# Kernel optimization log

Hardware: AMD Instinct MI355X
Metric: run time of the kernel (lower is better)

Reference implementation:

```python
import jax, jax.numpy as jnp
import numpy as np

B, T, C, H = 8, 2048, 1024, 64


def build_rope_cache(seq_len, dim):
    half = dim // 2
    inv_freq = 1.0 / (10000.0 ** (jnp.arange(half, dtype=jnp.float32) / half))
    t = jnp.arange(seq_len, dtype=jnp.float32)
    freqs = t[:, None] * inv_freq[None, :]          # (T, half)
    cos = jnp.repeat(jnp.cos(freqs), 2, axis=-1)    # (T, dim) interleaved
    sin = jnp.repeat(jnp.sin(freqs), 2, axis=-1)
    return cos, sin


def apply_rope(x, cos, sin):
    # x: (B, T, H); cos/sin: (T, H)
    x1 = x[..., ::2]
    x2 = x[..., 1::2]
    rot = jnp.stack([-x2, x1], axis=-1).reshape(x.shape)
    return x * cos[None] + rot * sin[None]


def setup_inputs() -> dict:
    key = jax.random.key(0)
    kx, kq, kk, kv = jax.random.split(key, 4)
    scale = 1.0 / np.sqrt(C)
    return {
        "x": jax.random.normal(kx, (B, T, C), dtype=jnp.float32),
        "Wq": jax.random.normal(kq, (C, H), dtype=jnp.float32) * scale,
        "Wk": jax.random.normal(kk, (C, H), dtype=jnp.float32) * scale,
        "Wv": jax.random.normal(kv, (C, H), dtype=jnp.float32) * scale,
    }


def reference(x, Wq, Wk, Wv):
    Bc, Tc, _ = x.shape
    head_size = Wq.shape[1]
    cos, sin = build_rope_cache(Tc, head_size)

    q = apply_rope(x @ Wq, cos, sin)   # (B, T, H)
    k = apply_rope(x @ Wk, cos, sin)   # (B, T, H)
    v = x @ Wv                          # (B, T, H)

    # full TxT masked softmax attention (matches original non-fused path)
    wei = jnp.einsum('bth,bsh->bts', q, k) * (head_size ** -0.5)  # (B, T, T)
    causal = jnp.tril(jnp.ones((Tc, Tc), dtype=bool))
    wei = jnp.where(causal[None], wei, -jnp.inf)
    wei = jax.nn.softmax(wei, axis=-1)
    # dropout p=0 (eval mode) -> identity
    return jnp.einsum('bts,bsh->bth', wei, v)
```

## Files before the change

### kernel.cpp

```cpp
#include <hip/hip_runtime.h>
#include <cmath>

#define Tn  2048
#define Cn  1024
#define Hn  64
#define BTn 16384

typedef _Float16 f16x8 __attribute__((ext_vector_type(8)));
typedef _Float16 f16x4 __attribute__((ext_vector_type(4)));
typedef _Float16 f16x2 __attribute__((ext_vector_type(2)));
typedef float    f32x4 __attribute__((ext_vector_type(4)));

__global__ __launch_bounds__(256) void prep_w_kernel(
    const float* __restrict__ Wq, const float* __restrict__ Wk,
    const float* __restrict__ Wv, _Float16* __restrict__ Wt)
{
    __shared__ float ts[64][65];
    const int blk = blockIdx.x;
    const int p   = blk >> 4;
    const int c0  = (blk & 15) * 64;
    const float* __restrict__ W = (p == 0) ? Wq : (p == 1) ? Wk : Wv;
    const int tid = threadIdx.x;
    #pragma unroll
    for (int it = 0; it < 16; it++) {
        int idx = tid + it * 256;
        int c = idx >> 6, n = idx & 63;
        ts[c][n] = W[(size_t)(c0 + c) * Hn + n];
    }
    __syncthreads();
    #pragma unroll
    for (int it = 0; it < 16; it++) {
        int idx = tid + it * 256;
        int n = idx >> 6, c = idx & 63;
        Wt[(size_t)(p * 64 + n) * Cn + c0 + c] = (_Float16)ts[c][n];
    }
}

#define XSP 1032

__global__ __launch_bounds__(512) void proj_kernel(
    const float* __restrict__ x, const _Float16* __restrict__ Wt,
    _Float16* __restrict__ qh, _Float16* __restrict__ kh, _Float16* __restrict__ vT)
{
    __shared__ _Float16 xs[32 * XSP];
    const int row0 = blockIdx.x * 32;
    const int tid  = threadIdx.x;
    const int wave = tid >> 6, lane = tid & 63;
    const int quad = lane >> 4, l15 = lane & 15;
    const int wr = wave >> 2, wc = wave & 3;

    #pragma unroll 8
    for (int it = 0; it < 16; it++) {
        int idx = tid + it * 512;
        int r = idx >> 8, c4 = idx & 255;
        float4 xv = *(const float4*)&x[(size_t)(row0 + r) * Cn + c4 * 4];
        f16x4 hv = { (_Float16)xv.x, (_Float16)xv.y, (_Float16)xv.z, (_Float16)xv.w };
        *(f16x4*)&xs[r * XSP + c4 * 4] = hv;
    }
    __syncthreads();

    f32x4 acc[3] = {};
    const _Float16* __restrict__ wb = Wt + (size_t)(wc * 48 + l15) * Cn + quad * 8;

    #pragma unroll 4
    for (int kc = 0; kc < Cn; kc += 32) {
        f16x8 b0 = *(const f16x8*)&wb[kc];
        f16x8 b1 = *(const f16x8*)&wb[16 * Cn + kc];
        f16x8 b2 = *(const f16x8*)&wb[32 * Cn + kc];
        f16x8 a  = *(const f16x8*)&xs[(wr * 16 + l15) * XSP + kc + quad * 8];
        acc[0] = __builtin_amdgcn_mfma_f32_16x16x32_f16(a, b0, acc[0], 0, 0, 0);
        acc[1] = __builtin_amdgcn_mfma_f32_16x16x32_f16(a, b1, acc[1], 0, 0, 0);
        acc[2] = __builtin_amdgcn_mfma_f32_16x16x32_f16(a, b2, acc[2], 0, 0, 0);
    }

    const int bidx = row0 >> 11;
    #pragma unroll
    for (int nt = 0; nt < 3; nt++) {
        const int n = wc * 48 + nt * 16 + l15;
        const int p = n >> 6;
        const int h = n & 63;
        if (p < 2) {
            _Float16* __restrict__ outb = (p == 0) ? qh : kh;
            const float invf = __expf(-0.2878231366242557f * (float)(h >> 1));
            #pragma unroll
            for (int r = 0; r < 4; r++) {
                int   row = row0 + wr * 16 + quad * 4 + r;
                float val = acc[nt][r];
                float partner = __shfl_xor(val, 1, 64);
                float ang = (float)(row & (Tn - 1)) * invf;
                float sv, cv;
                __sincosf(ang, &sv, &cv);
                float res = (h & 1) ? fmaf(val, cv,  partner * sv)
                                    : fmaf(val, cv, -partner * sv);
                if (p == 0) res *= 0.125f;
                float resn = __shfl_xor(res, 1, 64);
                if (!(l15 & 1)) {
                    f16x2 pk = { (_Float16)res, (_Float16)resn };
                    *(f16x2*)&outb[(size_t)row * Hn + h] = pk;
                }
            }
        } else {
            int t = (row0 & (Tn - 1)) + wr * 16 + quad * 4;
            f16x4 pv = { (_Float16)acc[nt][0], (_Float16)acc[nt][1],
                         (_Float16)acc[nt][2], (_Float16)acc[nt][3] };
            *(f16x4*)&vT[((size_t)bidx * Hn + h) * Tn + t] = pv;
        }
    }
}

#define PSP 72

__global__ __launch_bounds__(256) void attn_kernel(
    const _Float16* __restrict__ qh, const _Float16* __restrict__ kh,
    const _Float16* __restrict__ vT, float* __restrict__ out)
{
    __shared__ _Float16 ps[4][16 * PSP];
    __shared__ float ocomb[4][16][68];
    __shared__ float mlcomb[4][2][16];

    const int blk = blockIdx.x;
    const int b   = blk & 7;
    const int j   = blk >> 3;
    const int jm  = j & 31, g = j >> 5;
    const int qt  = (g == 0) ? (127 - jm)
                  : (g == 1) ? (64 + jm)
                  : (g == 2) ? (63 - jm) : jm;
    const int t0  = qt * 16;
    const int tid = threadIdx.x;
    const int w = tid >> 6, lane = tid & 63;
    const int quad = lane >> 4, l15 = lane & 15;

    const _Float16* __restrict__ qb = qh + (size_t)b * Tn * Hn;
    const _Float16* __restrict__ kb = kh + (size_t)b * Tn * Hn;
    const _Float16* __restrict__ vb = vT + (size_t)b * Hn * Tn;

    const f16x8 aq0 = *(const f16x8*)&qb[(size_t)(t0 + l15) * Hn +      quad * 8];
    const f16x8 aq1 = *(const f16x8*)&qb[(size_t)(t0 + l15) * Hn + 32 + quad * 8];

    const _Float16 one1 = (_Float16)1.0f;
    const f16x8 onesv = { one1, one1, one1, one1, one1, one1, one1, one1 };

    float m_run[4];
    f32x4 oacc[5] = {};
    #pragma unroll
    for (int r = 0; r < 4; r++) m_run[r] = -1e30f;

    const int nst = (t0 + 16 + 63) >> 6;
    for (int jt = w; jt < nst; jt += 4) {
        const int s0 = jt * 64;

        f16x8 kf[4][2];
        #pragma unroll
        for (int nt = 0; nt < 4; nt++) {
            const _Float16* kp = &kb[(size_t)(s0 + nt * 16 + l15) * Hn + quad * 8];
            kf[nt][0] = *(const f16x8*)kp;
            kf[nt][1] = *(const f16x8*)(kp + 32);
        }
        f32x4 sacc[4];
        #pragma unroll
        for (int nt = 0; nt < 4; nt++) {
            f32x4 z = {};
            z = __builtin_amdgcn_mfma_f32_16x16x32_f16(aq0, kf[nt][0], z, 0, 0, 0);
            z = __builtin_amdgcn_mfma_f32_16x16x32_f16(aq1, kf[nt][1], z, 0, 0, 0);
            sacc[nt] = z;
        }

        f16x8 vf[2][4];
        #pragma unroll
        for (int sc = 0; sc < 2; sc++)
            #pragma unroll
            for (int ht = 0; ht < 4; ht++)
                vf[sc][ht] = *(const f16x8*)&vb[(size_t)(ht * 16 + l15) * Tn
                                                + s0 + sc * 32 + quad * 8];

        if (jt == nst - 1) {
            #pragma unroll
            for (int nt = 0; nt < 4; nt++)
                #pragma unroll
                for (int r = 0; r < 4; r++) {
                    int scol = s0 + nt * 16 + l15;
                    int trow = t0 + quad * 4 + r;
                    if (scol > trow) sacc[nt][r] = -1e30f;
                }
        }

        float pr[4][4];
        #pragma unroll
        for (int r = 0; r < 4; r++) {
            float mx = fmaxf(fmaxf(sacc[0][r], sacc[1][r]),
                             fmaxf(sacc[2][r], sacc[3][r]));
            #pragma unroll
            for (int off = 1; off < 16; off <<= 1)
                mx = fmaxf(mx, __shfl_xor(mx, off, 64));
            float mnew  = fmaxf(m_run[r], mx);
            float alpha = __expf(m_run[r] - mnew);
            m_run[r] = mnew;
            #pragma unroll
            for (int nt = 0; nt < 4; nt++)
                pr[nt][r] = __expf(sacc[nt][r] - mnew);
            #pragma unroll
            for (int ht = 0; ht < 5; ht++)
                oacc[ht][r] = oacc[ht][r] * alpha;
        }

        #pragma unroll
        for (int nt = 0; nt < 4; nt++)
            #pragma unroll
            for (int r = 0; r < 4; r++) {
                float pv = pr[nt][r];
                float pn = __shfl_xor(pv, 1, 64);
                if (!(l15 & 1)) {
                    f16x2 pk = { (_Float16)pv, (_Float16)pn };
                    *(f16x2*)&ps[w][(quad * 4 + r) * PSP + nt * 16 + l15] = pk;
                }
            }

        #pragma unroll
        for (int sc = 0; sc < 2; sc++) {
            f16x8 ap = *(const f16x8*)&ps[w][l15 * PSP + sc * 32 + quad * 8];
            #pragma unroll
            for (int ht = 0; ht < 4; ht++)
                oacc[ht] = __builtin_amdgcn_mfma_f32_16x16x32_f16(ap, vf[sc][ht],
                                                                  oacc[ht], 0, 0, 0);
            oacc[4] = __builtin_amdgcn_mfma_f32_16x16x32_f16(ap, onesv,
                                                             oacc[4], 0, 0, 0);
        }
    }

    #pragma unroll
    for (int r = 0; r < 4; r++) {
        #pragma unroll
        for (int ht = 0; ht < 4; ht++)
            ocomb[w][quad * 4 + r][ht * 16 + l15] = oacc[ht][r];
        if (l15 == 0) {
            mlcomb[w][0][quad * 4 + r] = m_run[r];
            mlcomb[w][1][quad * 4 + r] = oacc[4][r];
        }
    }
    __syncthreads();

    #pragma unroll
    for (int it = 0; it < 4; it++) {
        int idx = tid + it * 256;
        int row = idx >> 6, h = idx & 63;
        float m0 = mlcomb[0][0][row], m1 = mlcomb[1][0][row];
        float m2 = mlcomb[2][0][row], m3 = mlcomb[3][0][row];
        float mm = fmaxf(fmaxf(m0, m1), fmaxf(m2, m3));
        float a0 = __expf(m0 - mm), a1 = __expf(m1 - mm);
        float a2 = __expf(m2 - mm), a3 = __expf(m3 - mm);
        float ll = mlcomb[0][1][row] * a0 + mlcomb[1][1][row] * a1
                 + mlcomb[2][1][row] * a2 + mlcomb[3][1][row] * a3;
        float ov = ocomb[0][row][h] * a0 + ocomb[1][row][h] * a1
                 + ocomb[2][row][h] * a2 + ocomb[3][row][h] * a3;
        out[((size_t)b * Tn + t0 + row) * Hn + h] = ov / ll;
    }
}

extern "C" void kernel_launch(void* const* d_in, const int* in_sizes, int n_in,
                              void* d_out, int out_size, void* d_ws, size_t ws_size,
                              hipStream_t stream) {
    const float* x  = (const float*)d_in[0];
    const float* Wq = (const float*)d_in[1];
    const float* Wk = (const float*)d_in[2];
    const float* Wv = (const float*)d_in[3];

    const size_t qkvN = (size_t)BTn * Hn;
    _Float16* qh = (_Float16*)d_ws;
    _Float16* kh = qh + qkvN;
    _Float16* vT = kh + qkvN;
    _Float16* Wt = vT + qkvN;

    prep_w_kernel<<<48, 256, 0, stream>>>(Wq, Wk, Wv, Wt);
    proj_kernel<<<BTn / 32, 512, 0, stream>>>(x, Wt, qh, kh, vT);
    attn_kernel<<<1024, 256, 0, stream>>>(qh, kh, vT, (float*)d_out);
}
```

Before: 178.9 us.

## Prefetch weights and K tiles into registers, simplify P store, add occupancy hints

The projection kernel now double-buffers its weight fragments in registers across 64-wide K steps, issuing the next step's loads before the current MFMAs. The attention kernel prefetches the next K tile for the wave before the V loads and softmax, so global latency overlaps compute. The P tile is written to shared memory as individual fp16 stores, removing the shuffle-and-pack step. Both kernels gain min-blocks-per-CU launch bound hints. The extra live registers or the forced register cap may cause spills, and the narrower stores raise the LDS write count.

```diff
diff --git a/kernel.cpp b/kernel.cpp
--- a/kernel.cpp
+++ b/kernel.cpp
@@ -38,7 +38,7 @@
 
 #define XSP 1032
 
-__global__ __launch_bounds__(512) void proj_kernel(
+__global__ __launch_bounds__(512, 4) void proj_kernel(
     const float* __restrict__ x, const _Float16* __restrict__ Wt,
     _Float16* __restrict__ qh, _Float16* __restrict__ kh, _Float16* __restrict__ vT)
 {
@@ -62,15 +62,33 @@
     f32x4 acc[3] = {};
     const _Float16* __restrict__ wb = Wt + (size_t)(wc * 48 + l15) * Cn + quad * 8;
 
-    #pragma unroll 4
-    for (int kc = 0; kc < Cn; kc += 32) {
-        f16x8 b0 = *(const f16x8*)&wb[kc];
-        f16x8 b1 = *(const f16x8*)&wb[16 * Cn + kc];
-        f16x8 b2 = *(const f16x8*)&wb[32 * Cn + kc];
-        f16x8 a  = *(const f16x8*)&xs[(wr * 16 + l15) * XSP + kc + quad * 8];
-        acc[0] = __builtin_amdgcn_mfma_f32_16x16x32_f16(a, b0, acc[0], 0, 0, 0);
-        acc[1] = __builtin_amdgcn_mfma_f32_16x16x32_f16(a, b1, acc[1], 0, 0, 0);
-        acc[2] = __builtin_amdgcn_mfma_f32_16x16x32_f16(a, b2, acc[2], 0, 0, 0);
+    f16x8 wbuf[2][3][2];
+    #pragma unroll
+    for (int nt = 0; nt < 3; nt++) {
+        wbuf[0][nt][0] = *(const f16x8*)&wb[nt * 16 * Cn];
+        wbuf[0][nt][1] = *(const f16x8*)&wb[nt * 16 * Cn + 32];
+    }
+
+    #pragma unroll 2
+    for (int ki = 0; ki < 16; ki++) {
+        const int cur = ki & 1;
+        if (ki < 15) {
+            const int kn = (ki + 1) * 64;
+            #pragma unroll
+            for (int nt = 0; nt < 3; nt++) {
+                wbuf[cur ^ 1][nt][0] = *(const f16x8*)&wb[nt * 16 * Cn + kn];
+                wbuf[cur ^ 1][nt][1] = *(const f16x8*)&wb[nt * 16 * Cn + kn + 32];
+            }
+        }
+        f16x8 a0 = *(const f16x8*)&xs[(wr * 16 + l15) * XSP + ki * 64 +      quad * 8];
+        f16x8 a1 = *(const f16x8*)&xs[(wr * 16 + l15) * XSP + ki * 64 + 32 + quad * 8];
+        #pragma unroll
+        for (int nt = 0; nt < 3; nt++) {
+            acc[nt] = __builtin_amdgcn_mfma_f32_16x16x32_f16(a0, wbuf[cur][nt][0],
+                                                             acc[nt], 0, 0, 0);
+            acc[nt] = __builtin_amdgcn_mfma_f32_16x16x32_f16(a1, wbuf[cur][nt][1],
+                                                             acc[nt], 0, 0, 0);
+        }
     }
 
     const int bidx = row0 >> 11;
@@ -110,7 +128,7 @@
 
 #define PSP 72
 
-__global__ __launch_bounds__(256) void attn_kernel(
+__global__ __launch_bounds__(256, 4) void attn_kernel(
     const _Float16* __restrict__ qh, const _Float16* __restrict__ kh,
     const _Float16* __restrict__ vT, float* __restrict__ out)
 {
@@ -146,16 +164,18 @@
     for (int r = 0; r < 4; r++) m_run[r] = -1e30f;
 
     const int nst = (t0 + 16 + 63) >> 6;
+
+    f16x8 kf[4][2];
+    #pragma unroll
+    for (int nt = 0; nt < 4; nt++) {
+        const _Float16* kp = &kb[(size_t)(w * 64 + nt * 16 + l15) * Hn + quad * 8];
+        kf[nt][0] = *(const f16x8*)kp;
+        kf[nt][1] = *(const f16x8*)(kp + 32);
+    }
+
     for (int jt = w; jt < nst; jt += 4) {
         const int s0 = jt * 64;
 
-        f16x8 kf[4][2];
-        #pragma unroll
-        for (int nt = 0; nt < 4; nt++) {
-            const _Float16* kp = &kb[(size_t)(s0 + nt * 16 + l15) * Hn + quad * 8];
-            kf[nt][0] = *(const f16x8*)kp;
-            kf[nt][1] = *(const f16x8*)(kp + 32);
-        }
         f32x4 sacc[4];
         #pragma unroll
         for (int nt = 0; nt < 4; nt++) {
@@ -163,6 +183,16 @@
             z = __builtin_amdgcn_mfma_f32_16x16x32_f16(aq0, kf[nt][0], z, 0, 0, 0);
             z = __builtin_amdgcn_mfma_f32_16x16x32_f16(aq1, kf[nt][1], z, 0, 0, 0);
             sacc[nt] = z;
+        }
+
+        if (jt + 4 < nst) {
+            const int sn = (jt + 4) * 64;
+            #pragma unroll
+            for (int nt = 0; nt < 4; nt++) {
+                const _Float16* kp = &kb[(size_t)(sn + nt * 16 + l15) * Hn + quad * 8];
+                kf[nt][0] = *(const f16x8*)kp;
+                kf[nt][1] = *(const f16x8*)(kp + 32);
+            }
         }
 
         f16x8 vf[2][4];
@@ -206,14 +236,8 @@
         #pragma unroll
         for (int nt = 0; nt < 4; nt++)
             #pragma unroll
-            for (int r = 0; r < 4; r++) {
-                float pv = pr[nt][r];
-                float pn = __shfl_xor(pv, 1, 64);
-                if (!(l15 & 1)) {
-                    f16x2 pk = { (_Float16)pv, (_Float16)pn };
-                    *(f16x2*)&ps[w][(quad * 4 + r) * PSP + nt * 16 + l15] = pk;
-                }
-            }
+            for (int r = 0; r < 4; r++)
+                ps[w][(quad * 4 + r) * PSP + nt * 16 + l15] = (_Float16)pr[nt][r];
 
         #pragma unroll
         for (int sc = 0; sc < 2; sc++) {
```

New measurement: 180.5 us. About the same (+0.9%).

## Stream x directly into projection MFMAs, prefetch K tiles, simplify P stores

Applied to the files above, without the earlier changes.

The projection kernel drops its LDS staging of x. It now uses 16-row blocks of 256 threads, and each wave loads fp32 x straight from global memory and converts it to fp16 in registers for the MFMA. The attention kernel gains an occupancy hint, loads the next K tile one iteration ahead to hide latency, and writes P to LDS as scalar fp16 stores instead of shuffle-packed pairs. Risks: x is re-read by all four waves with no LDS reuse, the prefetch raises register pressure, and the scalar LDS stores issue more instructions.

```diff
diff --git a/kernel.cpp b/kernel.cpp
--- a/kernel.cpp
+++ b/kernel.cpp
@@ -36,47 +36,38 @@
     }
 }
 
-#define XSP 1032
-
-__global__ __launch_bounds__(512) void proj_kernel(
+__global__ __launch_bounds__(256) void proj_kernel(
     const float* __restrict__ x, const _Float16* __restrict__ Wt,
     _Float16* __restrict__ qh, _Float16* __restrict__ kh, _Float16* __restrict__ vT)
 {
-    __shared__ _Float16 xs[32 * XSP];
-    const int row0 = blockIdx.x * 32;
+    const int row0 = blockIdx.x * 16;
     const int tid  = threadIdx.x;
     const int wave = tid >> 6, lane = tid & 63;
     const int quad = lane >> 4, l15 = lane & 15;
-    const int wr = wave >> 2, wc = wave & 3;
-
-    #pragma unroll 8
-    for (int it = 0; it < 16; it++) {
-        int idx = tid + it * 512;
-        int r = idx >> 8, c4 = idx & 255;
-        float4 xv = *(const float4*)&x[(size_t)(row0 + r) * Cn + c4 * 4];
-        f16x4 hv = { (_Float16)xv.x, (_Float16)xv.y, (_Float16)xv.z, (_Float16)xv.w };
-        *(f16x4*)&xs[r * XSP + c4 * 4] = hv;
-    }
-    __syncthreads();
+
+    const float*    __restrict__ xr = x  + (size_t)(row0 + l15) * Cn + quad * 8;
+    const _Float16* __restrict__ wb = Wt + (size_t)(wave * 48 + l15) * Cn + quad * 8;
 
     f32x4 acc[3] = {};
-    const _Float16* __restrict__ wb = Wt + (size_t)(wc * 48 + l15) * Cn + quad * 8;
 
     #pragma unroll 4
     for (int kc = 0; kc < Cn; kc += 32) {
+        float4 a0 = *(const float4*)&xr[kc];
+        float4 a1 = *(const float4*)&xr[kc + 4];
         f16x8 b0 = *(const f16x8*)&wb[kc];
         f16x8 b1 = *(const f16x8*)&wb[16 * Cn + kc];
         f16x8 b2 = *(const f16x8*)&wb[32 * Cn + kc];
-        f16x8 a  = *(const f16x8*)&xs[(wr * 16 + l15) * XSP + kc + quad * 8];
-        acc[0] = __builtin_amdgcn_mfma_f32_16x16x32_f16(a, b0, acc[0], 0, 0, 0);
-        acc[1] = __builtin_amdgcn_mfma_f32_16x16x32_f16(a, b1, acc[1], 0, 0, 0);
-        acc[2] = __builtin_amdgcn_mfma_f32_16x16x32_f16(a, b2, acc[2], 0, 0, 0);
+        f16x8 af = { (_Float16)a0.x, (_Float16)a0.y, (_Float16)a0.z, (_Float16)a0.w,
+                     (_Float16)a1.x, (_Float16)a1.y, (_Float16)a1.z, (_Float16)a1.w };
+        acc[0] = __builtin_amdgcn_mfma_f32_16x16x32_f16(af, b0, acc[0], 0, 0, 0);
+        acc[1] = __builtin_amdgcn_mfma_f32_16x16x32_f16(af, b1, acc[1], 0, 0, 0);
+        acc[2] = __builtin_amdgcn_mfma_f32_16x16x32_f16(af, b2, acc[2], 0, 0, 0);
     }
 
     const int bidx = row0 >> 11;
     #pragma unroll
     for (int nt = 0; nt < 3; nt++) {
-        const int n = wc * 48 + nt * 16 + l15;
+        const int n = wave * 48 + nt * 16 + l15;
         const int p = n >> 6;
         const int h = n & 63;
         if (p < 2) {
@@ -84,7 +75,7 @@
             const float invf = __expf(-0.2878231366242557f * (float)(h >> 1));
             #pragma unroll
             for (int r = 0; r < 4; r++) {
-                int   row = row0 + wr * 16 + quad * 4 + r;
+                int   row = row0 + quad * 4 + r;
                 float val = acc[nt][r];
                 float partner = __shfl_xor(val, 1, 64);
                 float ang = (float)(row & (Tn - 1)) * invf;
@@ -100,7 +91,7 @@
                 }
             }
         } else {
-            int t = (row0 & (Tn - 1)) + wr * 16 + quad * 4;
+            int t = (row0 & (Tn - 1)) + quad * 4;
             f16x4 pv = { (_Float16)acc[nt][0], (_Float16)acc[nt][1],
                          (_Float16)acc[nt][2], (_Float16)acc[nt][3] };
             *(f16x4*)&vT[((size_t)bidx * Hn + h) * Tn + t] = pv;
@@ -110,7 +101,7 @@
 
 #define PSP 72
 
-__global__ __launch_bounds__(256) void attn_kernel(
+__global__ __launch_bounds__(256, 4) void attn_kernel(
     const _Float16* __restrict__ qh, const _Float16* __restrict__ kh,
     const _Float16* __restrict__ vT, float* __restrict__ out)
 {
@@ -146,16 +137,18 @@
     for (int r = 0; r < 4; r++) m_run[r] = -1e30f;
 
     const int nst = (t0 + 16 + 63) >> 6;
+
+    f16x8 kf[4][2];
+    #pragma unroll
+    for (int nt = 0; nt < 4; nt++) {
+        const _Float16* kp = &kb[(size_t)(w * 64 + nt * 16 + l15) * Hn + quad * 8];
+        kf[nt][0] = *(const f16x8*)kp;
+        kf[nt][1] = *(const f16x8*)(kp + 32);
+    }
+
     for (int jt = w; jt < nst; jt += 4) {
         const int s0 = jt * 64;
 
-        f16x8 kf[4][2];
-        #pragma unroll
-        for (int nt = 0; nt < 4; nt++) {
-            const _Float16* kp = &kb[(size_t)(s0 + nt * 16 + l15) * Hn + quad * 8];
-            kf[nt][0] = *(const f16x8*)kp;
-            kf[nt][1] = *(const f16x8*)(kp + 32);
-        }
         f32x4 sacc[4];
         #pragma unroll
         for (int nt = 0; nt < 4; nt++) {
@@ -163,6 +156,16 @@
             z = __builtin_amdgcn_mfma_f32_16x16x32_f16(aq0, kf[nt][0], z, 0, 0, 0);
             z = __builtin_amdgcn_mfma_f32_16x16x32_f16(aq1, kf[nt][1], z, 0, 0, 0);
             sacc[nt] = z;
+        }
+
+        if (jt + 4 < nst) {
+            const int sn = (jt + 4) * 64;
+            #pragma unroll
+            for (int nt = 0; nt < 4; nt++) {
+                const _Float16* kp = &kb[(size_t)(sn + nt * 16 + l15) * Hn + quad * 8];
+                kf[nt][0] = *(const f16x8*)kp;
+                kf[nt][1] = *(const f16x8*)(kp + 32);
+            }
         }
 
         f16x8 vf[2][4];
@@ -206,14 +209,8 @@
         #pragma unroll
         for (int nt = 0; nt < 4; nt++)
             #pragma unroll
-            for (int r = 0; r < 4; r++) {
-                float pv = pr[nt][r];
-                float pn = __shfl_xor(pv, 1, 64);
-                if (!(l15 & 1)) {
-                    f16x2 pk = { (_Float16)pv, (_Float16)pn };
-                    *(f16x2*)&ps[w][(quad * 4 + r) * PSP + nt * 16 + l15] = pk;
-                }
-            }
+            for (int r = 0; r < 4; r++)
+                ps[w][(quad * 4 + r) * PSP + nt * 16 + l15] = (_Float16)pr[nt][r];
 
         #pragma unroll
         for (int sc = 0; sc < 2; sc++) {
@@ -271,6 +268,6 @@
     _Float16* Wt = vT + qkvN;
 
     prep_w_kernel<<<48, 256, 0, stream>>>(Wq, Wk, Wv, Wt);
-    proj_kernel<<<BTn / 32, 512, 0, stream>>>(x, Wt, qh, kh, vT);
+    proj_kernel<<<BTn / 16, 256, 0, stream>>>(x, Wt, qh, kh, vT);
     attn_kernel<<<1024, 256, 0, stream>>>(qh, kh, vT, (float*)d_out);
 }
```

Measured after the change: 199.8 us. +11.7%, slower.
